# Kernel tuning notes

Hardware: AMD Instinct MI355X
Metric: run time of the kernel (lower is better)

Reference implementation:

```python
import jax, jax.numpy as jnp
import numpy as np

MU = 0.5
SMALL_MASS_CUTOFF = 1e-10
NP_PART = 2_000_000
W = 8            # linear hex stencil, 2^3 nodes per particle
DIM = 3
NC = 2_097_152   # 128^3 grid cells
NS = 200_000     # selected boundary (level-set) nodes


def setup_inputs() -> dict:
    key = jax.random.key(0)
    k0, k1, k2, k3, k4, k5 = jax.random.split(key, 6)
    mass_stack = jax.random.uniform(k0, (NP_PART,), dtype=jnp.float32)
    shapef_grad_stack = jax.random.normal(k1, (NP_PART, W, DIM), dtype=jnp.float32)
    cnode_ids = jax.random.randint(k2, (NP_PART, W), 0, NC, dtype=jnp.int32)
    node_moment_nt = jax.random.normal(k3, (NC, DIM), dtype=jnp.float32)
    node_mass = jax.random.uniform(k4, (NC,), dtype=jnp.float32)
    id_stack = jnp.arange(NS, dtype=jnp.int32)  # unique selected node ids
    velocity_stack = jax.random.normal(k5, (NS, DIM), dtype=jnp.float32)
    return {
        "mass_stack": mass_stack,
        "shapef_grad_stack": shapef_grad_stack,
        "cnode_ids": cnode_ids,
        "node_moment_nt": node_moment_nt,
        "node_mass": node_mass,
        "id_stack": id_stack,
        "velocity_stack": velocity_stack,
    }


def reference(mass_stack, shapef_grad_stack, cnode_ids, node_moment_nt,
              node_mass, id_stack, velocity_stack):
    dim = velocity_stack.shape[-1]
    nc = node_mass.shape[0]

    # ---- P2G: accumulate mass-weighted shape-function gradients into grid normals
    # normal[c] += shapef_grad[p, w, :dim] * mass[p] for every (p, w) -> c = cnode_ids[p, w]
    contrib = shapef_grad_stack * mass_stack[:, None, None]           # [Np, W, dim]
    normal_stack = jax.ops.segment_sum(contrib.reshape(-1, dim),
                                       cnode_ids.reshape(-1),
                                       num_segments=nc)               # [NC, dim]

    # ---- per selected node friction update (vectorized over NS)
    normal = normal_stack[id_stack]          # [NS, dim]
    moment_nt = node_moment_nt[id_stack]     # [NS, dim]
    mass = node_mass[id_stack]               # [NS]

    valid = mass > SMALL_MASS_CUTOFF
    inv_mass = jnp.where(valid, 1.0 / jnp.where(valid, mass, 1.0), 0.0)
    vel_nt = moment_nt * inv_mass[:, None]   # cond(mass>cutoff, m/mass, 0)

    nnorm = jnp.sqrt(jnp.sum(normal * normal, axis=-1, keepdims=True))
    nrm_ok = valid[:, None] & (nnorm > 0)
    normal_hat = jnp.where(nrm_ok, normal / jnp.where(nnorm > 0, nnorm, 1.0), 0.0)

    delta_vel = vel_nt - velocity_stack                                # [NS, dim]
    dvn = jnp.sum(delta_vel * normal_hat, axis=-1)                     # [NS]

    cross = jnp.cross(delta_vel, normal_hat)                           # [NS, 3]
    cnorm = jnp.sqrt(jnp.sum(cross * cross, axis=-1))                  # [NS]
    omega = jnp.where((cnorm > 0)[:, None],
                      cross / jnp.where(cnorm > 0, cnorm, 1.0)[:, None], 0.0)
    mu_prime = jnp.minimum(MU, cnorm / jnp.where(dvn != 0, dvn, 1.0))  # only used when dvn>0
    tangent = normal_hat + mu_prime[:, None] * jnp.cross(normal_hat, omega)

    apply_fric = (dvn > 0.0)[:, None]
    new_vel_nt = jnp.where(apply_fric, vel_nt - dvn[:, None] * tangent, vel_nt)
    levelset_moment = new_vel_nt * mass[:, None]                       # [NS, dim]

    # ---- scatter-set back into the grid moment field
    return node_moment_nt.at[id_stack].set(levelset_moment)
```

## Files before the change

### kernel.cpp

```cpp
#include <hip/hip_runtime.h>


#define MU_F 0.5f
#define SMALL_MASS_CUTOFF 1e-10f

#define FP_SCALE 1048576.0f
#define FP_INV   9.5367431640625e-07f
#define FP_BIAS  (1 << 24)

typedef unsigned long long u64;
typedef unsigned int u32;

template <bool COMPACT>
__global__ void build_mask_kernel(const int* __restrict__ id_stack, int ns,
                                  u32* __restrict__ mask,
                                  u64* __restrict__ acc,
                                  u32* __restrict__ inv) {
    int i = blockIdx.x * blockDim.x + threadIdx.x;
    if (i >= ns) return;
    int id = id_stack[i];
    atomicOr(&mask[(u32)id >> 5], 1u << (id & 31));
    size_t slot = COMPACT ? (size_t)i : (size_t)id;
    if (COMPACT) inv[id] = (u32)i;
    acc[2 * slot]     = 0ull;
    acc[2 * slot + 1] = (u64)(u32)i << 40;
}

template <int LOG2W, bool COMPACT>
__global__ void p2g_kernel(const float* __restrict__ mass_stack,
                           const float* __restrict__ grad,
                           const int*   __restrict__ ids,
                           const u32*   __restrict__ mask,
                           const u32*   __restrict__ inv,
                           u64* __restrict__ acc,
                           int npairs, int W) {
    int pair = blockIdx.x * blockDim.x + threadIdx.x;
    if (pair >= npairs) return;
    int id = ids[pair];
    u32 mword = mask[(u32)id >> 5];
    if (mword & (1u << (id & 31))) {
        int pidx = (LOG2W > 0) ? (pair >> LOG2W) : (pair / W);
        float m = mass_stack[pidx];
        const float* g = grad + (size_t)pair * 3;
        int xi = __float2int_rn(g[0] * m * FP_SCALE);
        int yi = __float2int_rn(g[1] * m * FP_SCALE);
        int zi = __float2int_rn(g[2] * m * FP_SCALE);
        u64 a = ((u64)(u32)(yi + FP_BIAS) << 32) | (u32)(xi + FP_BIAS);
        u64 b = (1ull << 32) | (u32)(zi + FP_BIAS);
        size_t slot = COMPACT ? (size_t)inv[id] : (size_t)id;
        atomicAdd(&acc[2 * slot], a);
        atomicAdd(&acc[2 * slot + 1], b);
    }
}

template <bool COMPACT>
__global__ void epilogue_kernel(const float* __restrict__ node_moment,
                                const u32*   __restrict__ mask,
                                const u32*   __restrict__ inv,
                                const u64*   __restrict__ acc,
                                const float* __restrict__ node_mass,
                                const float* __restrict__ velocity,
                                float* __restrict__ out,
                                int nc) {
    int c = blockIdx.x * blockDim.x + threadIdx.x;
    if (c >= nc) return;
    size_t b3 = (size_t)c * 3;
    float mx = node_moment[b3 + 0];
    float my = node_moment[b3 + 1];
    float mz = node_moment[b3 + 2];

    u32 mword = mask[(u32)c >> 5];
    if (!(mword & (1u << (c & 31)))) {
        out[b3 + 0] = mx; out[b3 + 1] = my; out[b3 + 2] = mz;
        return;
    }

    size_t slot = COMPACT ? (size_t)inv[c] : (size_t)c;
    u64 a  = acc[2 * slot];
    u64 bb = acc[2 * slot + 1];
    u32 cnt = (u32)(bb >> 32) & 0xFFu;
    int i   = (int)(bb >> 40);
    long long bias = (long long)cnt * (long long)FP_BIAS;
    float nx = (float)((long long)(a & 0xFFFFFFFFull) - bias) * FP_INV;
    float ny = (float)((long long)(a >> 32) - bias) * FP_INV;
    float nz = (float)((long long)(bb & 0xFFFFFFFFull) - bias) * FP_INV;

    float mass = node_mass[c];
    bool valid = mass > SMALL_MASS_CUTOFF;
    float inv_mass = valid ? 1.0f / mass : 0.0f;
    float vx = mx * inv_mass, vy = my * inv_mass, vz = mz * inv_mass;

    float nn = sqrtf(nx * nx + ny * ny + nz * nz);
    bool ok = valid && (nn > 0.0f);
    float hx = 0.0f, hy = 0.0f, hz = 0.0f;
    if (ok) { float r = 1.0f / nn; hx = nx * r; hy = ny * r; hz = nz * r; }

    size_t vb = (size_t)i * 3;
    float dvx = vx - velocity[vb + 0];
    float dvy = vy - velocity[vb + 1];
    float dvz = vz - velocity[vb + 2];
    float dvn = dvx * hx + dvy * hy + dvz * hz;

    float ox = vx, oy = vy, oz = vz;
    if (dvn > 0.0f) {
        float cx = dvy * hz - dvz * hy;
        float cy = dvz * hx - dvx * hz;
        float cz = dvx * hy - dvy * hx;
        float cn = sqrtf(cx * cx + cy * cy + cz * cz);
        float wx = 0.0f, wy = 0.0f, wz = 0.0f;
        if (cn > 0.0f) { float r = 1.0f / cn; wx = cx * r; wy = cy * r; wz = cz * r; }
        float mu_p = fminf(MU_F, cn / dvn);
        float tx = hx + mu_p * (hy * wz - hz * wy);
        float ty = hy + mu_p * (hz * wx - hx * wz);
        float tz = hz + mu_p * (hx * wy - hy * wx);
        ox = vx - dvn * tx;
        oy = vy - dvn * ty;
        oz = vz - dvn * tz;
    }
    out[b3 + 0] = ox * mass;
    out[b3 + 1] = oy * mass;
    out[b3 + 2] = oz * mass;
}

extern "C" void kernel_launch(void* const* d_in, const int* in_sizes, int n_in,
                              void* d_out, int out_size, void* d_ws, size_t ws_size,
                              hipStream_t stream) {
    const float* mass_stack  = (const float*)d_in[0];
    const float* grad        = (const float*)d_in[1];
    const int*   cnode_ids   = (const int*)d_in[2];
    const float* node_moment = (const float*)d_in[3];
    const float* node_mass   = (const float*)d_in[4];
    const int*   id_stack    = (const int*)d_in[5];
    const float* velocity    = (const float*)d_in[6];
    float* out = (float*)d_out;

    const int np     = in_sizes[0];
    const int npairs = in_sizes[2];
    const int nc     = in_sizes[4];
    const int ns     = in_sizes[5];
    const int W      = npairs / np;

    const size_t mask_words = (size_t)(nc + 31) / 32;

    const size_t need_full    = (size_t)nc * 16 + mask_words * 4;
    const bool   compact      = ws_size < need_full;

    u64* acc;
    u32* inv;
    u32* mask;
    if (!compact) {
        acc  = (u64*)d_ws;
        mask = (u32*)(acc + 2 * (size_t)nc);
        inv  = nullptr;
    } else {
        acc  = (u64*)d_ws;
        inv  = (u32*)(acc + 2 * (size_t)ns);
        mask = inv + (size_t)nc;
    }

    (void)hipMemsetAsync(mask, 0, mask_words * 4, stream);

    const int mb = (ns + 255) / 256;
    const int pb = (npairs + 255) / 256;
    const int eb = (nc + 255) / 256;

    if (!compact) {
        build_mask_kernel<false><<<mb, 256, 0, stream>>>(id_stack, ns, mask, acc, inv);
        if (W == 8)
            p2g_kernel<3, false><<<pb, 256, 0, stream>>>(mass_stack, grad, cnode_ids,
                                                         mask, inv, acc, npairs, W);
        else if (W == 4)
            p2g_kernel<2, false><<<pb, 256, 0, stream>>>(mass_stack, grad, cnode_ids,
                                                         mask, inv, acc, npairs, W);
        else
            p2g_kernel<0, false><<<pb, 256, 0, stream>>>(mass_stack, grad, cnode_ids,
                                                         mask, inv, acc, npairs, W);
        epilogue_kernel<false><<<eb, 256, 0, stream>>>(node_moment, mask, inv, acc,
                                                       node_mass, velocity, out, nc);
    } else {
        build_mask_kernel<true><<<mb, 256, 0, stream>>>(id_stack, ns, mask, acc, inv);
        if (W == 8)
            p2g_kernel<3, true><<<pb, 256, 0, stream>>>(mass_stack, grad, cnode_ids,
                                                        mask, inv, acc, npairs, W);
        else if (W == 4)
            p2g_kernel<2, true><<<pb, 256, 0, stream>>>(mass_stack, grad, cnode_ids,
                                                        mask, inv, acc, npairs, W);
        else
            p2g_kernel<0, true><<<pb, 256, 0, stream>>>(mass_stack, grad, cnode_ids,
                                                        mask, inv, acc, npairs, W);
        epilogue_kernel<true><<<eb, 256, 0, stream>>>(node_moment, mask, inv, acc,
                                                      node_mass, velocity, out, nc);
    }
}
```

Before: 460.5 us.

## Replace inverse-index map with bitmask popcount rank for compact accumulator slots

Selected nodes now map to compact accumulator slots through a rank computed from the bitmask plus a per-word prefix sum (built by a single-block scan), replacing either the full-grid accumulator or the full-size inverse table. Velocities are also permuted into rank order so the epilogue reads them by slot. The compact accumulator and the rank array are far smaller than the full-grid or inverse-map layout, which should cut workspace traffic and improve cache hit rates for the atomics. In exchange it adds a serial-ish single-block scan over 65K mask words and two extra kernel launches.

```diff
diff --git a/kernel.cpp b/kernel.cpp
--- a/kernel.cpp
+++ b/kernel.cpp
@@ -11,27 +11,78 @@
 typedef unsigned long long u64;
 typedef unsigned int u32;
 
-template <bool COMPACT>
-__global__ void build_mask_kernel(const int* __restrict__ id_stack, int ns,
-                                  u32* __restrict__ mask,
-                                  u64* __restrict__ acc,
-                                  u32* __restrict__ inv) {
+__device__ __forceinline__ u32 rank_of(int id, u32 mword,
+                                       const u32* __restrict__ rankbase) {
+    return rankbase[(u32)id >> 5] + __popc(mword & ((1u << (id & 31)) - 1u));
+}
+
+__global__ void mask_kernel(const int* __restrict__ id_stack, int ns,
+                            u32* __restrict__ mask) {
     int i = blockIdx.x * blockDim.x + threadIdx.x;
     if (i >= ns) return;
     int id = id_stack[i];
     atomicOr(&mask[(u32)id >> 5], 1u << (id & 31));
-    size_t slot = COMPACT ? (size_t)i : (size_t)id;
-    if (COMPACT) inv[id] = (u32)i;
-    acc[2 * slot]     = 0ull;
-    acc[2 * slot + 1] = (u64)(u32)i << 40;
-}
-
-template <int LOG2W, bool COMPACT>
+}
+
+__global__ void scan_kernel(const u32* __restrict__ mask,
+                            u32* __restrict__ rankbase, int words) {
+    __shared__ u32 wave_sums[16];
+    const int t = threadIdx.x;
+    const int per = (words + 1023) / 1024;
+    const int w0 = t * per;
+    const int w1 = (w0 + per < words) ? (w0 + per) : words;
+
+    u32 local = 0;
+    for (int w = w0; w < w1; ++w) local += __popc(mask[w]);
+
+    u32 v = local;
+    const int lane = t & 63;
+    for (int d = 1; d < 64; d <<= 1) {
+        u32 u = __shfl_up(v, d);
+        if (lane >= d) v += u;
+    }
+    const int wid = t >> 6;
+    if (lane == 63) wave_sums[wid] = v;
+    __syncthreads();
+    if (t == 0) {
+        u32 run = 0;
+        for (int i = 0; i < 16; ++i) { u32 s = wave_sums[i]; wave_sums[i] = run; run += s; }
+    }
+    __syncthreads();
+
+    u32 excl = v - local + wave_sums[wid];
+    for (int w = w0; w < w1; ++w) {
+        rankbase[w] = excl;
+        excl += __popc(mask[w]);
+    }
+}
+
+__global__ void init_kernel(const int* __restrict__ id_stack,
+                            const float* __restrict__ velocity,
+                            const u32* __restrict__ mask,
+                            const u32* __restrict__ rankbase,
+                            u64* __restrict__ acc,
+                            float* __restrict__ vel_r,
+                            int ns) {
+    int i = blockIdx.x * blockDim.x + threadIdx.x;
+    if (i >= ns) return;
+    int id = id_stack[i];
+    u32 mword = mask[(u32)id >> 5];
+    u32 slot = rank_of(id, mword, rankbase);
+    acc[2 * (size_t)slot]     = 0ull;
+    acc[2 * (size_t)slot + 1] = 0ull;
+    size_t sb = (size_t)slot * 3, ib = (size_t)i * 3;
+    vel_r[sb + 0] = velocity[ib + 0];
+    vel_r[sb + 1] = velocity[ib + 1];
+    vel_r[sb + 2] = velocity[ib + 2];
+}
+
+template <int LOG2W>
 __global__ void p2g_kernel(const float* __restrict__ mass_stack,
                            const float* __restrict__ grad,
                            const int*   __restrict__ ids,
                            const u32*   __restrict__ mask,
-                           const u32*   __restrict__ inv,
+                           const u32*   __restrict__ rankbase,
                            u64* __restrict__ acc,
                            int npairs, int W) {
     int pair = blockIdx.x * blockDim.x + threadIdx.x;
@@ -47,19 +98,18 @@
         int zi = __float2int_rn(g[2] * m * FP_SCALE);
         u64 a = ((u64)(u32)(yi + FP_BIAS) << 32) | (u32)(xi + FP_BIAS);
         u64 b = (1ull << 32) | (u32)(zi + FP_BIAS);
-        size_t slot = COMPACT ? (size_t)inv[id] : (size_t)id;
-        atomicAdd(&acc[2 * slot], a);
-        atomicAdd(&acc[2 * slot + 1], b);
-    }
-}
-
-template <bool COMPACT>
+        u32 slot = rank_of(id, mword, rankbase);
+        atomicAdd(&acc[2 * (size_t)slot], a);
+        atomicAdd(&acc[2 * (size_t)slot + 1], b);
+    }
+}
+
 __global__ void epilogue_kernel(const float* __restrict__ node_moment,
                                 const u32*   __restrict__ mask,
-                                const u32*   __restrict__ inv,
+                                const u32*   __restrict__ rankbase,
                                 const u64*   __restrict__ acc,
                                 const float* __restrict__ node_mass,
-                                const float* __restrict__ velocity,
+                                const float* __restrict__ vel_r,
                                 float* __restrict__ out,
                                 int nc) {
     int c = blockIdx.x * blockDim.x + threadIdx.x;
@@ -75,14 +125,13 @@
         return;
     }
 
-    size_t slot = COMPACT ? (size_t)inv[c] : (size_t)c;
-    u64 a  = acc[2 * slot];
-    u64 bb = acc[2 * slot + 1];
-    u32 cnt = (u32)(bb >> 32) & 0xFFu;
-    int i   = (int)(bb >> 40);
-    long long bias = (long long)cnt * (long long)FP_BIAS;
-    float nx = (float)((long long)(a & 0xFFFFFFFFull) - bias) * FP_INV;
-    float ny = (float)((long long)(a >> 32) - bias) * FP_INV;
+    u32 slot = rank_of(c, mword, rankbase);
+    u64 a  = acc[2 * (size_t)slot];
+    u64 bb = acc[2 * (size_t)slot + 1];
+    u32 cnt = (u32)(bb >> 32);
+    long long bias = (long long)cnt << 24;
+    float nx = (float)((long long)(a  & 0xFFFFFFFFull) - bias) * FP_INV;
+    float ny = (float)((long long)(a  >> 32)           - bias) * FP_INV;
     float nz = (float)((long long)(bb & 0xFFFFFFFFull) - bias) * FP_INV;
 
     float mass = node_mass[c];
@@ -95,10 +144,10 @@
     float hx = 0.0f, hy = 0.0f, hz = 0.0f;
     if (ok) { float r = 1.0f / nn; hx = nx * r; hy = ny * r; hz = nz * r; }
 
-    size_t vb = (size_t)i * 3;
-    float dvx = vx - velocity[vb + 0];
-    float dvy = vy - velocity[vb + 1];
-    float dvz = vz - velocity[vb + 2];
+    size_t sb = (size_t)slot * 3;
+    float dvx = vx - vel_r[sb + 0];
+    float dvy = vy - vel_r[sb + 1];
+    float dvz = vz - vel_r[sb + 2];
     float dvn = dvx * hx + dvy * hy + dvz * hz;
 
     float ox = vx, oy = vy, oz = vz;
@@ -139,56 +188,32 @@
     const int nc     = in_sizes[4];
     const int ns     = in_sizes[5];
     const int W      = npairs / np;
-
-    const size_t mask_words = (size_t)(nc + 31) / 32;
-
-    const size_t need_full    = (size_t)nc * 16 + mask_words * 4;
-    const bool   compact      = ws_size < need_full;
-
-    u64* acc;
-    u32* inv;
-    u32* mask;
-    if (!compact) {
-        acc  = (u64*)d_ws;
-        mask = (u32*)(acc + 2 * (size_t)nc);
-        inv  = nullptr;
-    } else {
-        acc  = (u64*)d_ws;
-        inv  = (u32*)(acc + 2 * (size_t)ns);
-        mask = inv + (size_t)nc;
-    }
-
-    (void)hipMemsetAsync(mask, 0, mask_words * 4, stream);
+    const int words  = (nc + 31) / 32;
+
+    u64*   acc      = (u64*)d_ws;
+    float* vel_r    = (float*)(acc + 2 * (size_t)ns);
+    u32*   mask     = (u32*)(vel_r + 3 * (size_t)ns);
+    u32*   rankbase = mask + (size_t)words;
+
+    (void)hipMemsetAsync(mask, 0, (size_t)words * 4, stream);
 
     const int mb = (ns + 255) / 256;
     const int pb = (npairs + 255) / 256;
     const int eb = (nc + 255) / 256;
 
-    if (!compact) {
-        build_mask_kernel<false><<<mb, 256, 0, stream>>>(id_stack, ns, mask, acc, inv);
-        if (W == 8)
-            p2g_kernel<3, false><<<pb, 256, 0, stream>>>(mass_stack, grad, cnode_ids,
-                                                         mask, inv, acc, npairs, W);
-        else if (W == 4)
-            p2g_kernel<2, false><<<pb, 256, 0, stream>>>(mass_stack, grad, cnode_ids,
-                                                         mask, inv, acc, npairs, W);
-        else
-            p2g_kernel<0, false><<<pb, 256, 0, stream>>>(mass_stack, grad, cnode_ids,
-                                                         mask, inv, acc, npairs, W);
-        epilogue_kernel<false><<<eb, 256, 0, stream>>>(node_moment, mask, inv, acc,
-                                                       node_mass, velocity, out, nc);
-    } else {
-        build_mask_kernel<true><<<mb, 256, 0, stream>>>(id_stack, ns, mask, acc, inv);
-        if (W == 8)
-            p2g_kernel<3, true><<<pb, 256, 0, stream>>>(mass_stack, grad, cnode_ids,
-                                                        mask, inv, acc, npairs, W);
-        else if (W == 4)
-            p2g_kernel<2, true><<<pb, 256, 0, stream>>>(mass_stack, grad, cnode_ids,
-                                                        mask, inv, acc, npairs, W);
-        else
-            p2g_kernel<0, true><<<pb, 256, 0, stream>>>(mass_stack, grad, cnode_ids,
-                                                        mask, inv, acc, npairs, W);
-        epilogue_kernel<true><<<eb, 256, 0, stream>>>(node_moment, mask, inv, acc,
-                                                      node_mass, velocity, out, nc);
-    }
-}
+    mask_kernel<<<mb, 256, 0, stream>>>(id_stack, ns, mask);
+    scan_kernel<<<1, 1024, 0, stream>>>(mask, rankbase, words);
+    init_kernel<<<mb, 256, 0, stream>>>(id_stack, velocity, mask, rankbase,
+                                        acc, vel_r, ns);
+    if (W == 8)
+        p2g_kernel<3><<<pb, 256, 0, stream>>>(mass_stack, grad, cnode_ids,
+                                              mask, rankbase, acc, npairs, W);
+    else if (W == 4)
+        p2g_kernel<2><<<pb, 256, 0, stream>>>(mass_stack, grad, cnode_ids,
+                                              mask, rankbase, acc, npairs, W);
+    else
+        p2g_kernel<0><<<pb, 256, 0, stream>>>(mass_stack, grad, cnode_ids,
+                                              mask, rankbase, acc, npairs, W);
+    epilogue_kernel<<<eb, 256, 0, stream>>>(node_moment, mask, rankbase, acc,
+                                            node_mass, vel_r, out, nc);
+}
```

Measured after the change: 573.3 us. +24.5%, slower.
